# Kernel tuning notes

Hardware: AMD Instinct MI355X
Metric: run time of the kernel (lower is better)

Reference implementation:

```python
import jax, jax.numpy as jnp
import numpy as np

N = 10000
E = 160000
EPS = 1e-5


def _bn(x, g, b):
    # BatchNorm1d over node dim, training-mode batch stats, biased variance
    m = jnp.mean(x, axis=0)
    v = jnp.mean((x - m) ** 2, axis=0)
    return (x - m) * jax.lax.rsqrt(v + EPS) * g + b


def _graph_conv(x, src, dst, ew, w_rel, b_rel, w_root):
    # PyG GraphConv: lin_rel(scatter_add(ew * x[src] -> dst)) + lin_root(x)
    agg = jax.ops.segment_sum(x[src] * ew[:, None], dst, num_segments=N)
    return agg @ w_rel + b_rel + x @ w_root


def setup_inputs() -> dict:
    key = jax.random.key(0)
    ks = jax.random.split(key, 16)
    x = jax.random.normal(ks[0], (N, 517), jnp.float32)
    edge_index = jax.random.randint(ks[1], (2, E), 0, N, dtype=jnp.int64)
    edge_weight = jax.random.uniform(ks[2], (E,), jnp.float32)

    def lin(k, fi, fo):
        return jax.random.normal(k, (fi, fo), jnp.float32) / np.sqrt(fi)

    d = dict(x=x, edge_index=edge_index, edge_weight=edge_weight)
    dims = [(517, 256), (256, 128), (128, 64)]
    for i, (fi, fo) in enumerate(dims, 1):
        d[f"w_rel{i}"] = lin(ks[3 * i], fi, fo)
        d[f"b_rel{i}"] = jnp.zeros((fo,), jnp.float32)
        d[f"w_root{i}"] = lin(ks[3 * i + 1], fi, fo)
        d[f"bn{i}_g"] = jnp.ones((fo,), jnp.float32)
        d[f"bn{i}_b"] = jnp.zeros((fo,), jnp.float32)
    d["w_lin"] = lin(ks[13], 64, 1)
    d["b_lin"] = jnp.zeros((1,), jnp.float32)
    return d


def reference(x, edge_index, edge_weight,
              w_rel1, b_rel1, w_root1, bn1_g, bn1_b,
              w_rel2, b_rel2, w_root2, bn2_g, bn2_b,
              w_rel3, b_rel3, w_root3, bn3_g, bn3_b,
              w_lin, b_lin):
    src, dst = edge_index[0], edge_index[1]
    h = jax.nn.relu(_bn(_graph_conv(x, src, dst, edge_weight, w_rel1, b_rel1, w_root1), bn1_g, bn1_b))
    h = jax.nn.relu(_bn(_graph_conv(h, src, dst, edge_weight, w_rel2, b_rel2, w_root2), bn2_g, bn2_b))
    h = jax.nn.relu(_bn(_graph_conv(h, src, dst, edge_weight, w_rel3, b_rel3, w_root3), bn3_g, bn3_b))
    h = jax.nn.log_sigmoid(h @ w_lin + b_lin)           # [N, 1]
    norm = jax.scipy.special.logsumexp(h, axis=0)        # [1]
    return h - norm
```

## Files before the change

### kernel.cpp

```cpp
#include <hip/hip_runtime.h>
#include <math.h>

#define NN 10000
#define EE 160000
#define MP 10112
#define EPSBN 1e-5f

typedef __attribute__((ext_vector_type(8))) short short8;
typedef __attribute__((ext_vector_type(4))) short short4v;
typedef __attribute__((ext_vector_type(4))) float f32x4;

__device__ __forceinline__ short f2bf(float f) {
    union { float f; unsigned u; } v; v.f = f;
    unsigned r = v.u + 0x7FFF + ((v.u >> 16) & 1);
    return (short)(r >> 16);
}
__device__ __forceinline__ float bf2f(unsigned short u) {
    union { unsigned u; float f; } v; v.u = ((unsigned)u) << 16;
    return v.f;
}
__device__ __forceinline__ void gload16(const short* g, short* l) {
    __builtin_amdgcn_global_load_lds((const __attribute__((address_space(1))) void*)g,
                                     (__attribute__((address_space(3))) void*)l, 16, 0, 0);
}


__global__ void count_kernel(const int* __restrict__ dst, int* __restrict__ deg, int E) {
    int e = blockIdx.x * blockDim.x + threadIdx.x;
    if (e < E) atomicAdd(&deg[dst[e]], 1);
}

__global__ __launch_bounds__(1024) void scan_kernel(const int* __restrict__ deg, int* __restrict__ off,
                                                    int* __restrict__ cursor, int n) {
    __shared__ int sm[1024];
    const int C = 10;
    int t = threadIdx.x;
    int base = t * C;
    int loc[C];
    int acc = 0;
#pragma unroll
    for (int i = 0; i < C; i++) {
        int idx = base + i;
        int v = (idx < n) ? deg[idx] : 0;
        loc[i] = acc;
        acc += v;
    }
    sm[t] = acc;
    __syncthreads();
    for (int d = 1; d < 1024; d <<= 1) {
        int v = (t >= d) ? sm[t - d] : 0;
        __syncthreads();
        sm[t] += v;
        __syncthreads();
    }
    int prefix = (t > 0) ? sm[t - 1] : 0;
#pragma unroll
    for (int i = 0; i < C; i++) {
        int idx = base + i;
        if (idx < n) {
            int o = prefix + loc[i];
            off[idx] = o;
            cursor[idx] = o;
        }
    }
    if (t == 1023) off[n] = sm[1023];
}

__global__ void fill_kernel(const int* __restrict__ src, const int* __restrict__ dst,
                            const float* __restrict__ ew, int* __restrict__ cursor,
                            int* __restrict__ psrc, float* __restrict__ pew, int E) {
    int e = blockIdx.x * blockDim.x + threadIdx.x;
    if (e < E) {
        int d = dst[e];
        int slot = atomicAdd(&cursor[d], 1);
        psrc[slot] = src[e];
        pew[slot] = ew[e];
    }
}


__global__ void conv_x_kernel(const float* __restrict__ x, short* __restrict__ A) {
    int idx = blockIdx.x * 256 + threadIdx.x;
    if (idx >= MP * 72) return;
    int row = idx / 72;
    int c0 = (idx % 72) * 8;
    short8 s;
    bool gr = (row < NN);
#pragma unroll
    for (int j = 0; j < 8; j++) {
        int c = c0 + j;
        float v = (gr && c < 517) ? x[(size_t)row * 517 + c] : 0.f;
        s[j] = f2bf(v);
    }
    *(short8*)&A[(size_t)row * 576 + c0] = s;
}


__global__ void conv_w_all(const float* __restrict__ w1r, const float* __restrict__ w1o,
                           const float* __restrict__ w2r, const float* __restrict__ w2o,
                           const float* __restrict__ w3r, const float* __restrict__ w3o,
                           short* __restrict__ B1, short* __restrict__ B2, short* __restrict__ B3) {
    int j = blockIdx.x;
    const float *Wr, *Wo;
    short* Bt;
    int K, Kp, fo, row;
    if (j < 512)      { row = j;       Wr = w1r; Wo = w1o; Bt = B1; K = 517; Kp = 576; fo = 256; }
    else if (j < 768) { row = j - 512; Wr = w2r; Wo = w2o; Bt = B2; K = 256; Kp = 256; fo = 128; }
    else              { row = j - 768; Wr = w3r; Wo = w3o; Bt = B3; K = 128; Kp = 128; fo = 64; }
    const float* W = (row < fo) ? Wr : Wo;
    int col = (row < fo) ? row : row - fo;
    for (int k = threadIdx.x; k < Kp; k += 256) {
        short v = 0;
        if (k < K) v = f2bf(W[(size_t)k * fo + col]);
        Bt[(size_t)row * Kp + k] = v;
    }
}


template <int MODE, int BM, int BN, int NT>
__global__ __launch_bounds__(NT) void mfma_gemm(const short* __restrict__ Abf,
                                                const float* __restrict__ Af32,
                                                const short* __restrict__ Bt,
                                                short* __restrict__ Yrel,
                                                float* __restrict__ Hroot,
                                                const float* __restrict__ brel,
                                                const float* __restrict__ ssum,
                                                const float* __restrict__ ssumsq,
                                                const float* __restrict__ bng,
                                                const float* __restrict__ bnb,
                                                int K, int Kp, int fo) {
    const int N_REP = BN / 16;
    const int ACH = BM * 8 / NT;
    const int BCH = BN * 8 / NT;
    const int AF4 = BM * 16 / NT;

    __shared__ short Als[2][BM * 64];
    __shared__ short Bls[2][BN * 64];
    __shared__ float scs[256], shs[256];

    int m0 = blockIdx.x * BM;
    int n0 = blockIdx.y * BN;
    int t = threadIdx.x;
    int lane = t & 63;
    int wid = t >> 6;

    if (MODE == 1) {
        for (int f = t; f < K; f += NT) {
            float mean = ssum[f] / (float)NN;
            float var = ssumsq[f] / (float)NN - mean * mean;
            var = fmaxf(var, 0.f);
            float sc = bng[f] * rsqrtf(var + EPSBN);
            scs[f] = sc;
            shs[f] = bnb[f] - mean * sc;
        }
        __syncthreads();
    }

    f32x4 acc[N_REP];
#pragma unroll
    for (int j = 0; j < N_REP; j++) acc[j] = (f32x4){0.f, 0.f, 0.f, 0.f};

    f32x4 ld[AF4 > 0 ? AF4 : 1];

    auto stageB = [&](int buf, int k0) {
#pragma unroll
        for (int i = 0; i < BCH; i++) {
            int idx = i * NT + t;
            int row = idx >> 3;
            int pc = idx & 7;
            gload16(Bt + (size_t)(n0 + row) * Kp + k0 + ((pc ^ (row & 7)) << 3), &Bls[buf][idx << 3]);
        }
    };
    auto stageA0 = [&](int buf, int k0) {
#pragma unroll
        for (int i = 0; i < ACH; i++) {
            int idx = i * NT + t;
            int row = idx >> 3;
            int pc = idx & 7;
            gload16(Abf + (size_t)(m0 + row) * Kp + k0 + ((pc ^ (row & 7)) << 3), &Als[buf][idx << 3]);
        }
    };
    auto loadA1 = [&](int k0) {
#pragma unroll
        for (int i = 0; i < AF4; i++) {
            int idx = i * NT + t;
            int row = idx >> 4;
            int fc = idx & 15;
            ld[i] = *(const f32x4*)(Af32 + (size_t)(m0 + row) * K + k0 + (fc << 2));
        }
    };
    auto writeA1 = [&](int buf, int k0) {
#pragma unroll
        for (int i = 0; i < AF4; i++) {
            int idx = i * NT + t;
            int row = idx >> 4;
            int fc = idx & 15;
            int kb = k0 + (fc << 2);
            short4v s;
#pragma unroll
            for (int j = 0; j < 4; j++) s[j] = f2bf(fmaxf(0.f, ld[i][j] * scs[kb + j] + shs[kb + j]));
            *(short4v*)&Als[buf][row * 64 + (((fc >> 1) ^ (row & 7)) << 3) + ((fc & 1) << 2)] = s;
        }
    };
    auto compute = [&](int buf) {
#pragma unroll
        for (int kk = 0; kk < 2; kk++) {
            int cc = kk * 4 + (lane >> 4);
            short8 af;
            {
                int row = wid * 16 + (lane & 15);
                af = *(const short8*)&Als[buf][(row * 8 + (cc ^ (row & 7))) * 8];
            }
#pragma unroll
            for (int ni = 0; ni < N_REP; ni++) {
                int row = ni * 16 + (lane & 15);
                short8 b8 = *(const short8*)&Bls[buf][(row * 8 + (cc ^ (row & 7))) * 8];
                acc[ni] = __builtin_amdgcn_mfma_f32_16x16x32_bf16(af, b8, acc[ni], 0, 0, 0);
            }
        }
    };

    int nsteps = Kp / 64;
    if (MODE == 0) stageA0(0, 0);
    else { loadA1(0); writeA1(0, 0); }
    stageB(0, 0);
    __syncthreads();

    int cur = 0;
    for (int s = 0; s < nsteps; s++) {
        int k1 = (s + 1) * 64;
        bool nxt = (s + 1 < nsteps);
        if (nxt) {
            if (MODE == 0) stageA0(cur ^ 1, k1);
            else loadA1(k1);
            stageB(cur ^ 1, k1);
        }
        compute(cur);
        if (nxt && MODE == 1) writeA1(cur ^ 1, k1);
        __syncthreads();
        cur ^= 1;
    }

#pragma unroll
    for (int ni = 0; ni < N_REP; ni++) {
        int gn = n0 + ni * 16 + (lane & 15);
        int row0 = m0 + wid * 16 + (lane >> 4) * 4;
        f32x4 v = acc[ni];
        if (gn < fo) {
#pragma unroll
            for (int r = 0; r < 4; r++) Yrel[(size_t)(row0 + r) * fo + gn] = f2bf(v[r]);
        } else {
            float bb = brel[gn - fo];
#pragma unroll
            for (int r = 0; r < 4; r++) Hroot[(size_t)(row0 + r) * fo + (gn - fo)] = v[r] + bb;
        }
    }
}


template <int FO>
__global__ __launch_bounds__(256) void agg_kernel(const short* __restrict__ Yrel,
                                                  float* __restrict__ hio,
                                                  const int* __restrict__ off,
                                                  const int* __restrict__ psrc,
                                                  const float* __restrict__ pew) {
    const int G = FO / 2;
    const int NPB = 256 / G;
    int t = threadIdx.x;
    int g = t / G;
    int tf = t % G;
    int f = tf * 2;
    int n = blockIdx.x * NPB + g;
    if (n >= NN) return;

    float a0 = 0.f, a1 = 0.f;
    int e0 = off[n], e1 = off[n + 1];
    int e = e0;
    for (; e + 1 < e1; e += 2) {
        int s0i = psrc[e], s1i = psrc[e + 1];
        float w0 = pew[e], w1 = pew[e + 1];
        unsigned p0 = *(const unsigned*)(Yrel + (size_t)s0i * FO + f);
        unsigned p1 = *(const unsigned*)(Yrel + (size_t)s1i * FO + f);
        a0 += w0 * bf2f((unsigned short)(p0 & 0xffff));
        a1 += w0 * bf2f((unsigned short)(p0 >> 16));
        a0 += w1 * bf2f((unsigned short)(p1 & 0xffff));
        a1 += w1 * bf2f((unsigned short)(p1 >> 16));
    }
    if (e < e1) {
        int s0i = psrc[e];
        float w0 = pew[e];
        unsigned p0 = *(const unsigned*)(Yrel + (size_t)s0i * FO + f);
        a0 += w0 * bf2f((unsigned short)(p0 & 0xffff));
        a1 += w0 * bf2f((unsigned short)(p0 >> 16));
    }
    size_t o = (size_t)n * FO + f;
    hio[o]     += a0;
    hio[o + 1] += a1;
}


template <int FO>
__global__ __launch_bounds__(256) void stats_part(const float* __restrict__ hio,
                                                  float* __restrict__ pS,
                                                  float* __restrict__ pQ) {
    const int FG = FO / 4;
    const int ROWL = 256 / FG;
    const int RPB = (NN + 255) / 256;
    __shared__ f32x4 sms[256], smq[256];
    int t = threadIdx.x;
    int fg = t % FG;
    int rl = t / FG;
    int r0 = blockIdx.x * RPB;
    int r1 = r0 + RPB;
    if (r1 > NN) r1 = NN;
    f32x4 s = (f32x4){0.f, 0.f, 0.f, 0.f};
    f32x4 q = (f32x4){0.f, 0.f, 0.f, 0.f};
    for (int r = r0 + rl; r < r1; r += ROWL) {
        f32x4 v = *(const f32x4*)(hio + (size_t)r * FO + fg * 4);
        s += v;
        q += v * v;
    }
    sms[t] = s;
    smq[t] = q;
    __syncthreads();
    if (rl == 0) {
#pragma unroll
        for (int l = 1; l < ROWL; l++) {
            s += sms[l * FG + fg];
            q += smq[l * FG + fg];
        }
        *(f32x4*)(pS + (size_t)blockIdx.x * FO + fg * 4) = s;
        *(f32x4*)(pQ + (size_t)blockIdx.x * FO + fg * 4) = q;
    }
}

__global__ __launch_bounds__(256) void stats_reduce(const float* __restrict__ pS,
                                                    const float* __restrict__ pQ,
                                                    float* __restrict__ ssum,
                                                    float* __restrict__ ssumsq,
                                                    int FO) {
    int f = blockIdx.x;
    int t = threadIdx.x;
    float s = pS[(size_t)t * FO + f];
    float q = pQ[(size_t)t * FO + f];
#pragma unroll
    for (int o = 32; o > 0; o >>= 1) {
        s += __shfl_down(s, o, 64);
        q += __shfl_down(q, o, 64);
    }
    __shared__ float smS[4], smQ[4];
    int lane = t & 63, w = t >> 6;
    if (lane == 0) { smS[w] = s; smQ[w] = q; }
    __syncthreads();
    if (t == 0) {
        ssum[f]   = smS[0] + smS[1] + smS[2] + smS[3];
        ssumsq[f] = smQ[0] + smQ[1] + smQ[2] + smQ[3];
    }
}


__global__ void head_kernel(const float* __restrict__ hio,
                            const float* __restrict__ ssum, const float* __restrict__ ssumsq,
                            const float* __restrict__ g3, const float* __restrict__ b3,
                            const float* __restrict__ wlin, const float* __restrict__ blin,
                            float* __restrict__ tmp) {
    int lane = threadIdx.x & 63;
    int wv = threadIdx.x >> 6;
    int n = blockIdx.x * 4 + wv;
    float mean = ssum[lane] / (float)NN;
    float var = ssumsq[lane] / (float)NN - mean * mean;
    var = fmaxf(var, 0.f);
    float sc = g3[lane] * rsqrtf(var + EPSBN);
    float sh = b3[lane] - mean * sc;
    float v = fmaxf(0.f, hio[(size_t)n * 64 + lane] * sc + sh);
    float p = v * wlin[lane];
#pragma unroll
    for (int o = 32; o > 0; o >>= 1) p += __shfl_down(p, o, 64);
    if (lane == 0) {
        float x = p + blin[0];
        float ls = (x >= 0.f) ? (-log1pf(expf(-x))) : (x - log1pf(expf(x)));
        tmp[n] = ls;
    }
}


__global__ __launch_bounds__(1024) void lse_final(const float* __restrict__ tmp, float* __restrict__ out) {
    __shared__ float sm[1024];
    int t = threadIdx.x;
    float m = -INFINITY;
    for (int i = t; i < NN; i += 1024) m = fmaxf(m, tmp[i]);
    sm[t] = m;
    __syncthreads();
    for (int s = 512; s > 0; s >>= 1) {
        if (t < s) sm[t] = fmaxf(sm[t], sm[t + s]);
        __syncthreads();
    }
    float M = sm[0];
    __syncthreads();
    float acc = 0.f;
    for (int i = t; i < NN; i += 1024) acc += expf(tmp[i] - M);
    sm[t] = acc;
    __syncthreads();
    for (int s = 512; s > 0; s >>= 1) {
        if (t < s) sm[t] += sm[t + s];
        __syncthreads();
    }
    float L = M + logf(sm[0]);
    for (int i = t; i < NN; i += 1024) out[i] = tmp[i] - L;
}


extern "C" void kernel_launch(void* const* d_in, const int* in_sizes, int n_in,
                              void* d_out, int out_size, void* d_ws, size_t ws_size,
                              hipStream_t stream) {
    const float* x  = (const float*)d_in[0];
    const int* ei   = (const int*)d_in[1];
    const float* ew = (const float*)d_in[2];
    const int* src = ei;
    const int* dst = ei + EE;

    const float* wrel[3]  = { (const float*)d_in[3],  (const float*)d_in[8],  (const float*)d_in[13] };
    const float* brel[3]  = { (const float*)d_in[4],  (const float*)d_in[9],  (const float*)d_in[14] };
    const float* wroot[3] = { (const float*)d_in[5],  (const float*)d_in[10], (const float*)d_in[15] };
    const float* bng[3]   = { (const float*)d_in[6],  (const float*)d_in[11], (const float*)d_in[16] };
    const float* bnb[3]   = { (const float*)d_in[7],  (const float*)d_in[12], (const float*)d_in[17] };
    const float* wlin = (const float*)d_in[18];
    const float* blin = (const float*)d_in[19];
    float* out = (float*)d_out;

    char* p = (char*)d_ws;
    auto alloc = [&](size_t bytes) { char* r = p; p += (bytes + 255) & ~(size_t)255; return r; };

    int*   deg     = (int*)alloc(NN * 4);
    float* ssumAll = (float*)alloc(1536 * 4);
    int*   off     = (int*)alloc((NN + 4) * 4);
    int*   cursor  = (int*)alloc(NN * 4);
    int*   psrc    = (int*)alloc(EE * 4);
    float* pew     = (float*)alloc(EE * 4);
    short* A1      = (short*)alloc((size_t)MP * 576 * 2);
    short* B1t     = (short*)alloc((size_t)512 * 576 * 2);
    short* B2t     = (short*)alloc((size_t)256 * 256 * 2);
    short* B3t     = (short*)alloc((size_t)128 * 128 * 2);
    short* Yrel    = (short*)alloc((size_t)MP * 256 * 2);
    float* hA      = (float*)alloc((size_t)MP * 256 * 4);
    float* hB      = (float*)alloc((size_t)MP * 128 * 4);
    float* hC      = (float*)alloc((size_t)MP * 64 * 4);
    float* tmp     = (float*)alloc(NN * 4);
    float* pS      = (float*)alloc((size_t)256 * 256 * 4);
    float* pQ      = (float*)alloc((size_t)256 * 256 * 4);

    float* ss[3]  = { ssumAll,       ssumAll + 512,  ssumAll + 1024 };
    float* sq[3]  = { ssumAll + 256, ssumAll + 768,  ssumAll + 1280 };

    hipMemsetAsync(deg, 0, (size_t)((char*)(ssumAll + 1536) - (char*)deg), stream);

    count_kernel<<<(EE + 255) / 256, 256, 0, stream>>>(dst, deg, EE);
    scan_kernel<<<1, 1024, 0, stream>>>(deg, off, cursor, NN);
    fill_kernel<<<(EE + 255) / 256, 256, 0, stream>>>(src, dst, ew, cursor, psrc, pew, EE);
    conv_x_kernel<<<(MP * 72 + 255) / 256, 256, 0, stream>>>(x, A1);
    conv_w_all<<<896, 256, 0, stream>>>(wrel[0], wroot[0], wrel[1], wroot[1], wrel[2], wroot[2],
                                        B1t, B2t, B3t);

    mfma_gemm<0, 128, 128, 512><<<dim3(MP / 128, 4), 512, 0, stream>>>(
        A1, nullptr, B1t, Yrel, hA, brel[0], nullptr, nullptr, nullptr, nullptr, 576, 576, 256);
    agg_kernel<256><<<5000, 256, 0, stream>>>(Yrel, hA, off, psrc, pew);
    stats_part<256><<<256, 256, 0, stream>>>(hA, pS, pQ);
    stats_reduce<<<256, 256, 0, stream>>>(pS, pQ, ss[0], sq[0], 256);

    mfma_gemm<1, 64, 128, 256><<<dim3(MP / 64, 2), 256, 0, stream>>>(
        nullptr, hA, B2t, Yrel, hB, brel[1], ss[0], sq[0], bng[0], bnb[0], 256, 256, 128);
    agg_kernel<128><<<2500, 256, 0, stream>>>(Yrel, hB, off, psrc, pew);
    stats_part<128><<<256, 256, 0, stream>>>(hB, pS, pQ);
    stats_reduce<<<128, 256, 0, stream>>>(pS, pQ, ss[1], sq[1], 128);

    mfma_gemm<1, 64, 64, 256><<<dim3(MP / 64, 2), 256, 0, stream>>>(
        nullptr, hB, B3t, Yrel, hC, brel[2], ss[1], sq[1], bng[1], bnb[1], 128, 128, 64);
    agg_kernel<64><<<1250, 256, 0, stream>>>(Yrel, hC, off, psrc, pew);
    stats_part<64><<<256, 256, 0, stream>>>(hC, pS, pQ);
    stats_reduce<<<64, 256, 0, stream>>>(pS, pQ, ss[2], sq[2], 64);

    head_kernel<<<2500, 256, 0, stream>>>(hC, ss[2], sq[2], bng[2], bnb[2], wlin, blin, tmp);
    lse_final<<<1, 1024, 0, stream>>>(tmp, out);
}
```

Before: 176.5 us.

## Fuse prep kernels into one launch, unroll aggregation by four, shrink layer-1 GEMM tiles

Merges the x conversion, weight conversion and degree-count kernels into one multi-role prep launch, cutting two kernel launches and letting the independent work overlap. The aggregation loop is unrolled to four edges with two accumulator pairs, which puts more gather loads in flight at once. The first GEMM moves from 128x128 tiles with 512 threads to 64x128 tiles with 256 threads, doubling the block count for better CU occupancy at the cost of less operand reuse per block. Changing the accumulation order slightly alters floating-point rounding.

Result: faster. 157.4 us (-10.8%).

```diff
diff --git a/kernel.cpp b/kernel.cpp
--- a/kernel.cpp
+++ b/kernel.cpp
@@ -25,10 +25,48 @@
 }
 
 
-__global__ void count_kernel(const int* __restrict__ dst, int* __restrict__ deg, int E) {
-    int e = blockIdx.x * blockDim.x + threadIdx.x;
-    if (e < E) atomicAdd(&deg[dst[e]], 1);
-}
+__global__ __launch_bounds__(256) void prep_kernel(const float* __restrict__ x, short* __restrict__ A,
+                                                   const float* __restrict__ w1r, const float* __restrict__ w1o,
+                                                   const float* __restrict__ w2r, const float* __restrict__ w2o,
+                                                   const float* __restrict__ w3r, const float* __restrict__ w3o,
+                                                   short* __restrict__ B1, short* __restrict__ B2, short* __restrict__ B3,
+                                                   const int* __restrict__ dst, int* __restrict__ deg) {
+    int b = blockIdx.x;
+    if (b < 2848) {
+        int idx = b * 256 + threadIdx.x;
+        if (idx >= MP * 72) return;
+        int row = idx / 72;
+        int c0 = (idx % 72) * 8;
+        short8 s;
+        bool gr = (row < NN);
+#pragma unroll
+        for (int j = 0; j < 8; j++) {
+            int c = c0 + j;
+            float v = (gr && c < 517) ? x[(size_t)row * 517 + c] : 0.f;
+            s[j] = f2bf(v);
+        }
+        *(short8*)&A[(size_t)row * 576 + c0] = s;
+    } else if (b < 3744) {
+        int j = b - 2848;
+        const float *Wr, *Wo;
+        short* Bt;
+        int K, Kp, fo, row;
+        if (j < 512)      { row = j;       Wr = w1r; Wo = w1o; Bt = B1; K = 517; Kp = 576; fo = 256; }
+        else if (j < 768) { row = j - 512; Wr = w2r; Wo = w2o; Bt = B2; K = 256; Kp = 256; fo = 128; }
+        else              { row = j - 768; Wr = w3r; Wo = w3o; Bt = B3; K = 128; Kp = 128; fo = 64; }
+        const float* W = (row < fo) ? Wr : Wo;
+        int col = (row < fo) ? row : row - fo;
+        for (int k = threadIdx.x; k < Kp; k += 256) {
+            short v = 0;
+            if (k < K) v = f2bf(W[(size_t)k * fo + col]);
+            Bt[(size_t)row * Kp + k] = v;
+        }
+    } else {
+        int e = (b - 3744) * 256 + threadIdx.x;
+        if (e < EE) atomicAdd(&deg[dst[e]], 1);
+    }
+}
+
 
 __global__ __launch_bounds__(1024) void scan_kernel(const int* __restrict__ deg, int* __restrict__ off,
                                                     int* __restrict__ cursor, int n) {
@@ -75,44 +113,6 @@
         int slot = atomicAdd(&cursor[d], 1);
         psrc[slot] = src[e];
         pew[slot] = ew[e];
-    }
-}
-
-
-__global__ void conv_x_kernel(const float* __restrict__ x, short* __restrict__ A) {
-    int idx = blockIdx.x * 256 + threadIdx.x;
-    if (idx >= MP * 72) return;
-    int row = idx / 72;
-    int c0 = (idx % 72) * 8;
-    short8 s;
-    bool gr = (row < NN);
-#pragma unroll
-    for (int j = 0; j < 8; j++) {
-        int c = c0 + j;
-        float v = (gr && c < 517) ? x[(size_t)row * 517 + c] : 0.f;
-        s[j] = f2bf(v);
-    }
-    *(short8*)&A[(size_t)row * 576 + c0] = s;
-}
-
-
-__global__ void conv_w_all(const float* __restrict__ w1r, const float* __restrict__ w1o,
-                           const float* __restrict__ w2r, const float* __restrict__ w2o,
-                           const float* __restrict__ w3r, const float* __restrict__ w3o,
-                           short* __restrict__ B1, short* __restrict__ B2, short* __restrict__ B3) {
-    int j = blockIdx.x;
-    const float *Wr, *Wo;
-    short* Bt;
-    int K, Kp, fo, row;
-    if (j < 512)      { row = j;       Wr = w1r; Wo = w1o; Bt = B1; K = 517; Kp = 576; fo = 256; }
-    else if (j < 768) { row = j - 512; Wr = w2r; Wo = w2o; Bt = B2; K = 256; Kp = 256; fo = 128; }
-    else              { row = j - 768; Wr = w3r; Wo = w3o; Bt = B3; K = 128; Kp = 128; fo = 64; }
-    const float* W = (row < fo) ? Wr : Wo;
-    int col = (row < fo) ? row : row - fo;
-    for (int k = threadIdx.x; k < Kp; k += 256) {
-        short v = 0;
-        if (k < K) v = f2bf(W[(size_t)k * fo + col]);
-        Bt[(size_t)row * Kp + k] = v;
     }
 }
 
@@ -273,20 +273,26 @@
     int n = blockIdx.x * NPB + g;
     if (n >= NN) return;
 
-    float a0 = 0.f, a1 = 0.f;
+    float a0 = 0.f, a1 = 0.f, b0 = 0.f, b1 = 0.f;
     int e0 = off[n], e1 = off[n + 1];
     int e = e0;
-    for (; e + 1 < e1; e += 2) {
-        int s0i = psrc[e], s1i = psrc[e + 1];
-        float w0 = pew[e], w1 = pew[e + 1];
+    for (; e + 3 < e1; e += 4) {
+        int s0i = psrc[e], s1i = psrc[e + 1], s2i = psrc[e + 2], s3i = psrc[e + 3];
+        float w0 = pew[e], w1 = pew[e + 1], w2 = pew[e + 2], w3 = pew[e + 3];
         unsigned p0 = *(const unsigned*)(Yrel + (size_t)s0i * FO + f);
         unsigned p1 = *(const unsigned*)(Yrel + (size_t)s1i * FO + f);
+        unsigned p2 = *(const unsigned*)(Yrel + (size_t)s2i * FO + f);
+        unsigned p3 = *(const unsigned*)(Yrel + (size_t)s3i * FO + f);
         a0 += w0 * bf2f((unsigned short)(p0 & 0xffff));
         a1 += w0 * bf2f((unsigned short)(p0 >> 16));
-        a0 += w1 * bf2f((unsigned short)(p1 & 0xffff));
-        a1 += w1 * bf2f((unsigned short)(p1 >> 16));
-    }
-    if (e < e1) {
+        b0 += w1 * bf2f((unsigned short)(p1 & 0xffff));
+        b1 += w1 * bf2f((unsigned short)(p1 >> 16));
+        a0 += w2 * bf2f((unsigned short)(p2 & 0xffff));
+        a1 += w2 * bf2f((unsigned short)(p2 >> 16));
+        b0 += w3 * bf2f((unsigned short)(p3 & 0xffff));
+        b1 += w3 * bf2f((unsigned short)(p3 >> 16));
+    }
+    for (; e < e1; e++) {
         int s0i = psrc[e];
         float w0 = pew[e];
         unsigned p0 = *(const unsigned*)(Yrel + (size_t)s0i * FO + f);
@@ -294,8 +300,8 @@
         a1 += w0 * bf2f((unsigned short)(p0 >> 16));
     }
     size_t o = (size_t)n * FO + f;
-    hio[o]     += a0;
-    hio[o + 1] += a1;
+    hio[o]     += a0 + b0;
+    hio[o + 1] += a1 + b1;
 }
 
 
@@ -454,14 +460,13 @@
 
     hipMemsetAsync(deg, 0, (size_t)((char*)(ssumAll + 1536) - (char*)deg), stream);
 
-    count_kernel<<<(EE + 255) / 256, 256, 0, stream>>>(dst, deg, EE);
+    prep_kernel<<<4369, 256, 0, stream>>>(x, A1,
+                                          wrel[0], wroot[0], wrel[1], wroot[1], wrel[2], wroot[2],
+                                          B1t, B2t, B3t, dst, deg);
     scan_kernel<<<1, 1024, 0, stream>>>(deg, off, cursor, NN);
     fill_kernel<<<(EE + 255) / 256, 256, 0, stream>>>(src, dst, ew, cursor, psrc, pew, EE);
-    conv_x_kernel<<<(MP * 72 + 255) / 256, 256, 0, stream>>>(x, A1);
-    conv_w_all<<<896, 256, 0, stream>>>(wrel[0], wroot[0], wrel[1], wroot[1], wrel[2], wroot[2],
-                                        B1t, B2t, B3t);
-
-    mfma_gemm<0, 128, 128, 512><<<dim3(MP / 128, 4), 512, 0, stream>>>(
+
+    mfma_gemm<0, 64, 128, 256><<<dim3(MP / 64, 4), 256, 0, stream>>>(
         A1, nullptr, B1t, Yrel, hA, brel[0], nullptr, nullptr, nullptr, nullptr, 576, 576, 256);
     agg_kernel<256><<<5000, 256, 0, stream>>>(Yrel, hA, off, psrc, pew);
     stats_part<256><<<256, 256, 0, stream>>>(hA, pS, pQ);
```
